# Kernel tuning notes

Hardware: AMD Instinct MI355X
Metric: run time of the kernel (lower is better)

Reference implementation:

```python
import jax, jax.numpy as jnp
import numpy as np

B, L, E, H = 1, 4096, 1024, 16
D = E // H
EPS = 1e-6


def setup_inputs() -> dict:
    key = jax.random.key(0)
    k1, k2, k3 = jax.random.split(key, 3)
    # fan-in scaled init to keep activations sane
    x = jax.random.normal(k1, (B, L, E), dtype=jnp.float32)
    qkv_w = jax.random.normal(k2, (E, 3 * E), dtype=jnp.float32) / np.sqrt(E)
    qkv_b = jnp.zeros((3 * E,), dtype=jnp.float32)
    out_w = jax.random.normal(k3, (E, E), dtype=jnp.float32) / np.sqrt(E)
    out_b = jnp.zeros((E,), dtype=jnp.float32)
    return {"x": x, "qkv_w": qkv_w, "qkv_b": qkv_b, "out_w": out_w, "out_b": out_b}


def reference(x, qkv_w, qkv_b, out_w, out_b):
    b, l, e = x.shape
    qkv = x @ qkv_w + qkv_b                      # (B, L, 3E)
    q, k, v = jnp.split(qkv, 3, axis=-1)
    # (B, L, E) -> (B, H, L, D)
    q = q.reshape(b, l, H, D).transpose(0, 2, 1, 3)
    k = k.reshape(b, l, H, D).transpose(0, 2, 1, 3)
    v = v.reshape(b, l, H, D).transpose(0, 2, 1, 3)
    q_prime = jax.nn.elu(q) + 1.0
    k_prime = jax.nn.elu(k) + 1.0
    # cumulative sum of per-position outer products k'_l v_l^T : (B,H,L,D,D)
    kv_prod = jnp.einsum('bhld,bhle->bhlde', k_prime, v)
    kv_cumsum = jnp.cumsum(kv_prod, axis=2)
    context = jnp.einsum('bhld,bhlde->bhle', q_prime, kv_cumsum)  # (B,H,L,D)
    k_cumsum = jnp.cumsum(k_prime, axis=2)                        # (B,H,L,D)
    norm = jnp.einsum('bhld,bhld->bhl', q_prime, k_cumsum)        # (B,H,L)
    output = context / (norm[..., None] + EPS)
    output = output.transpose(0, 2, 1, 3).reshape(b, l, e)
    return output @ out_w + out_b
```

## Files before the change

### kernel.cpp

```cpp
#include <hip/hip_runtime.h>
#include <cstddef>
#include <cstdint>

#define L_SEQ 4096
#define EMB   1024
#define NH    16
#define HD    64
#define N3    3072
#define CHUNK 64
#define NCHUNK 64
#define EPS 1e-6f

typedef __attribute__((ext_vector_type(8))) short   bf16x8;
typedef __attribute__((ext_vector_type(4))) short   bf16x4;
typedef __attribute__((ext_vector_type(4))) float   floatx4;

#define AS1 __attribute__((address_space(1)))
#define AS3 __attribute__((address_space(3)))

__device__ __forceinline__ void gload_lds16(const void* g, void* l) {
    __builtin_amdgcn_global_load_lds((AS1 const unsigned int*)g,
                                     (AS3 unsigned int*)l, 16, 0, 0);
}

__device__ __forceinline__ short f2bf(float f) {
    union { float f; unsigned u; } a; a.f = f;
    unsigned r = a.u + 0x7fffu + ((a.u >> 16) & 1u);
    return (short)(r >> 16);
}
__device__ __forceinline__ float bf2f(short s) {
    union { unsigned u; float f; } a; a.u = ((unsigned)(unsigned short)s) << 16;
    return a.f;
}

__device__ __forceinline__ void transpose_tile(const float* __restrict__ W,
                                               short* __restrict__ WT,
                                               int K, int N, int bx, int by,
                                               float (*t)[65], int tid)
{
    const int r  = tid >> 4;
    const int c4 = (tid & 15) << 2;
#pragma unroll
    for (int s = 0; s < 4; ++s) {
        const int k = r + s * 16;
        const floatx4 v = *(const floatx4*)&W[(size_t)(by * 64 + k) * N + bx * 64 + c4];
        t[k][c4 + 0] = v[0]; t[k][c4 + 1] = v[1];
        t[k][c4 + 2] = v[2]; t[k][c4 + 3] = v[3];
    }
    __syncthreads();
#pragma unroll
    for (int s = 0; s < 4; ++s) {
        const int n = r + s * 16;
        bf16x4 o;
        o[0] = f2bf(t[c4 + 0][n]); o[1] = f2bf(t[c4 + 1][n]);
        o[2] = f2bf(t[c4 + 2][n]); o[3] = f2bf(t[c4 + 3][n]);
        *(bf16x4*)&WT[(size_t)(bx * 64 + n) * K + by * 64 + c4] = o;
    }
}

__global__ __launch_bounds__(256)
void prep(const float* __restrict__ x, short* __restrict__ xb,
          const float* __restrict__ qkv_w, short* __restrict__ qwt,
          const float* __restrict__ out_w, short* __restrict__ owt)
{
    __shared__ float t[64][65];
    const int b = blockIdx.x;
    const int tid = threadIdx.x;
    if (b < 2048) {
        const int i = b * 256 + tid;
        const floatx4 a = *(const floatx4*)(x + (size_t)i * 8);
        const floatx4 c = *(const floatx4*)(x + (size_t)i * 8 + 4);
        bf16x8 o;
        o[0] = f2bf(a[0]); o[1] = f2bf(a[1]); o[2] = f2bf(a[2]); o[3] = f2bf(a[3]);
        o[4] = f2bf(c[0]); o[5] = f2bf(c[1]); o[6] = f2bf(c[2]); o[7] = f2bf(c[3]);
        *(bf16x8*)(xb + (size_t)i * 8) = o;
    } else if (b < 2048 + 768) {
        const int u = b - 2048;
        transpose_tile(qkv_w, qwt, EMB, N3, u % 48, u / 48, t, tid);
    } else {
        const int u = b - 2816;
        transpose_tile(out_w, owt, EMB, EMB, u & 15, u >> 4, t, tid);
    }
}

#define CST 136

template<int MODE>
__global__ __launch_bounds__(256)
void mfma_gemm(const short* __restrict__ A, const short* __restrict__ BT,
               const float* __restrict__ bias,
               short* __restrict__ OQ, short* __restrict__ OK, short* __restrict__ OV,
               float* __restrict__ OF, int N, int K)
{
    __shared__ __align__(16) short smem[128 * CST];
    short* Asm = smem;
    short* Bsm = smem + 4096;
    const int tid  = threadIdx.x;
    const int lane = tid & 63;
    const int wave = tid >> 6;
    const int wm = (wave >> 1) * 64;
    const int wn = (wave & 1) * 64;
    const int bx = blockIdx.x;
    const int by = blockIdx.y;
    const int frow = lane & 15;
    const int fko  = (lane >> 4) << 3;

    const short* Ab = A  + (size_t)(by * 128) * K;
    const short* Bb = BT + (size_t)(bx * 128) * K;

    floatx4 acc[4][4] = {};

    for (int k0 = 0; k0 < K; k0 += 32) {
#pragma unroll
        for (int q = 0; q < 2; ++q) {
            const int ia = q * 256 + tid;
            const int row = ia >> 2;
            const int kc  = (ia & 3) << 3;
            gload_lds16(Ab + (size_t)row * K + k0 + kc, &Asm[ia << 3]);
            gload_lds16(Bb + (size_t)row * K + k0 + kc, &Bsm[ia << 3]);
        }
        __syncthreads();
        bf16x8 af[4], bfv[4];
#pragma unroll
        for (int mi = 0; mi < 4; ++mi)
            af[mi] = *(const bf16x8*)&Asm[(wm + mi * 16 + frow) * 32 + fko];
#pragma unroll
        for (int ni = 0; ni < 4; ++ni)
            bfv[ni] = *(const bf16x8*)&Bsm[(wn + ni * 16 + frow) * 32 + fko];
#pragma unroll
        for (int mi = 0; mi < 4; ++mi)
#pragma unroll
            for (int ni = 0; ni < 4; ++ni)
                acc[mi][ni] = __builtin_amdgcn_mfma_f32_16x16x32_bf16(
                    af[mi], bfv[ni], acc[mi][ni], 0, 0, 0);
        __syncthreads();
    }

    const int rq = (lane >> 4) << 2;
    if (MODE == 0) {
#pragma unroll
        for (int ni = 0; ni < 4; ++ni) {
            const int n = bx * 128 + wn + ni * 16 + frow;
            const float bv = bias[n];
            const bool do_elu = (n >> 10) < 2;
#pragma unroll
            for (int mi = 0; mi < 4; ++mi)
#pragma unroll
                for (int r = 0; r < 4; ++r) {
                    float v = acc[mi][ni][r] + bv;
                    if (do_elu) v = (v > 0.f) ? (v + 1.f) : __expf(v);
                    smem[(wm + mi * 16 + rq + r) * CST + wn + ni * 16 + frow] = f2bf(v);
                }
        }
        __syncthreads();
#pragma unroll
        for (int t = 0; t < 8; ++t) {
            const int idx = t * 256 + tid;
            const int mm = idx >> 4;
            const int c8 = (idx & 15) << 3;
            const bf16x8 val = *(const bf16x8*)&smem[mm * CST + c8];
            const int n0 = bx * 128 + c8;
            const int rsel = n0 >> 10;
            const int h  = (n0 & 1023) >> 6;
            const int d  = n0 & 63;
            short* base = (rsel == 0) ? OQ : (rsel == 1 ? OK : OV);
            *(bf16x8*)&base[((size_t)(h * L_SEQ + by * 128 + mm)) * HD + d] = val;
        }
    } else {
#pragma unroll
        for (int ni = 0; ni < 4; ++ni) {
            const int n = bx * 128 + wn + ni * 16 + frow;
            const float bv = bias[n];
#pragma unroll
            for (int mi = 0; mi < 4; ++mi)
#pragma unroll
                for (int r = 0; r < 4; ++r) {
                    const int m = by * 128 + wm + mi * 16 + rq + r;
                    OF[(size_t)m * N + n] = acc[mi][ni][r] + bv;
                }
        }
    }
}

__global__ __launch_bounds__(256)
void chunk_state(const short* __restrict__ Kb, const short* __restrict__ Vb,
                 short* __restrict__ ScTb, float* __restrict__ zc)
{
    __shared__ float Kc[CHUNK * HD];
    __shared__ float Vc[CHUNK * HD];
    const int c = blockIdx.x, h = blockIdx.y;
    const int tid = threadIdx.x;
    const short* Kg = Kb + ((size_t)h * L_SEQ + (size_t)c * CHUNK) * HD;
    const short* Vg = Vb + ((size_t)h * L_SEQ + (size_t)c * CHUNK) * HD;
#pragma unroll
    for (int q = 0; q < 2; ++q) {
        const int idx = q * 256 + tid;
        const bf16x8 kv = *(const bf16x8*)&Kg[idx * 8];
        const bf16x8 vv = *(const bf16x8*)&Vg[idx * 8];
#pragma unroll
        for (int j = 0; j < 8; ++j) {
            Kc[idx * 8 + j] = bf2f(kv[j]);
            Vc[idx * 8 + j] = bf2f(vv[j]);
        }
    }
    __syncthreads();
    const int e0 = (tid >> 4) << 2;
    const int d0 = (tid & 15) << 2;
    float acc[4][4] = {{0.f}};
    for (int l = 0; l < CHUNK; ++l) {
        const floatx4 ve = *(const floatx4*)&Vc[l * HD + e0];
        const floatx4 kd = *(const floatx4*)&Kc[l * HD + d0];
#pragma unroll
        for (int a = 0; a < 4; ++a)
#pragma unroll
            for (int b = 0; b < 4; ++b)
                acc[a][b] += ve[a] * kd[b];
    }
    short* Sout = ScTb + (size_t)(h * NCHUNK + c) * 4096;
#pragma unroll
    for (int a = 0; a < 4; ++a) {
        bf16x4 o;
        o[0] = f2bf(acc[a][0]); o[1] = f2bf(acc[a][1]);
        o[2] = f2bf(acc[a][2]); o[3] = f2bf(acc[a][3]);
        *(bf16x4*)&Sout[(e0 + a) * HD + d0] = o;
    }
    if (tid < HD) {
        float z = 0.f;
        for (int l = 0; l < CHUNK; ++l) z += Kc[l * HD + tid];
        zc[((size_t)(h * NCHUNK + c)) * HD + tid] = z;
    }
}

__global__ __launch_bounds__(256)
void prefix_scan(const short* __restrict__ ScTb, const float* __restrict__ zc,
                 short* __restrict__ S0b)
{
    const int g = blockIdx.x * 256 + threadIdx.x;
    const int h  = g >> 12;
    const int ed = g & 4095;
    const int e  = ed >> 6;
    const int d  = ed & 63;
    const short* src = ScTb + (size_t)h * NCHUNK * 4096 + ed;
    float run = 0.f;
    for (int cb = 0; cb < NCHUNK; cb += 8) {
        short v[8];
#pragma unroll
        for (int u = 0; u < 8; ++u) v[u] = src[(size_t)(cb + u) * 4096];
#pragma unroll
        for (int u = 0; u < 8; ++u) {
            S0b[((size_t)((h * NCHUNK + cb + u) * 65 + e)) * 64 + d] = f2bf(run);
            run += bf2f(v[u]);
        }
    }
    if (g < NH * HD) {
        const int h2 = g >> 6, d2 = g & 63;
        float rz = 0.f;
        for (int cb = 0; cb < NCHUNK; cb += 8) {
            float w[8];
#pragma unroll
            for (int u = 0; u < 8; ++u)
                w[u] = zc[((size_t)(h2 * NCHUNK + cb + u)) * HD + d2];
#pragma unroll
            for (int u = 0; u < 8; ++u) {
                S0b[((size_t)((h2 * NCHUNK + cb + u) * 65 + 64)) * 64 + d2] = f2bf(rz);
                rz += w[u];
            }
        }
    }
}

#define SP 72

__global__ __launch_bounds__(256)
void chunk_attn(const short* __restrict__ Qb, const short* __restrict__ Kb,
                const short* __restrict__ Vb, const short* __restrict__ S0b,
                short* __restrict__ attn)
{
    __shared__ __align__(16) short Qs[64 * SP];
    __shared__ __align__(16) short Ks[64 * SP];
    __shared__ __align__(16) short As[64 * SP];
    __shared__ __align__(16) short Vs[80 * SP];
    __shared__ __align__(16) short Ss[80 * SP];
    const int c = blockIdx.x, h = blockIdx.y;
    const int tid = threadIdx.x, lane = tid & 63, wave = tid >> 6;
    const size_t rb = ((size_t)h * L_SEQ + (size_t)c * CHUNK) * HD;
    const short* Qg = Qb + rb;
    const short* Kg = Kb + rb;
    const short* Vg = Vb + rb;
    const short* Sg = S0b + (size_t)(h * NCHUNK + c) * 65 * 64;

#pragma unroll
    for (int q = 0; q < 2; ++q) {
        const int idx = q * 256 + tid;
        const int row = idx >> 3, c8 = (idx & 7) << 3;
        *(bf16x8*)&Qs[row * SP + c8] = *(const bf16x8*)&Qg[row * 64 + c8];
        *(bf16x8*)&Ks[row * SP + c8] = *(const bf16x8*)&Kg[row * 64 + c8];
        const bf16x8 vv = *(const bf16x8*)&Vg[row * 64 + c8];
#pragma unroll
        for (int j = 0; j < 8; ++j) Vs[(c8 + j) * SP + row] = vv[j];
    }
    if (tid < 64) Vs[64 * SP + tid] = (short)0x3F80;
    for (int idx = tid; idx < 520; idx += 256) {
        const int row = idx >> 3, c8 = (idx & 7) << 3;
        *(bf16x8*)&Ss[row * SP + c8] = *(const bf16x8*)&Sg[row * 64 + c8];
    }
    __syncthreads();

    const int frow = lane & 15;
    const int quad = lane >> 4;
    const int fko  = quad << 3;
    const int wm   = wave << 4;

    const bf16x8 qf0 = *(const bf16x8*)&Qs[(wm + frow) * SP + fko];
    const bf16x8 qf1 = *(const bf16x8*)&Qs[(wm + frow) * SP + 32 + fko];

    floatx4 sacc[4] = {};
#pragma unroll
    for (int n = 0; n < 4; ++n) {
        const bf16x8 kf0 = *(const bf16x8*)&Ks[(n * 16 + frow) * SP + fko];
        const bf16x8 kf1 = *(const bf16x8*)&Ks[(n * 16 + frow) * SP + 32 + fko];
        sacc[n] = __builtin_amdgcn_mfma_f32_16x16x32_bf16(qf0, kf0, sacc[n], 0, 0, 0);
        sacc[n] = __builtin_amdgcn_mfma_f32_16x16x32_bf16(qf1, kf1, sacc[n], 0, 0, 0);
    }
#pragma unroll
    for (int n = 0; n < 4; ++n)
#pragma unroll
        for (int r = 0; r < 4; ++r) {
            const int i = wm + quad * 4 + r;
            const int j = n * 16 + frow;
            As[i * SP + j] = (j <= i) ? f2bf(sacc[n][r]) : (short)0;
        }
    __syncthreads();

    const bf16x8 af0 = *(const bf16x8*)&As[(wm + frow) * SP + fko];
    const bf16x8 af1 = *(const bf16x8*)&As[(wm + frow) * SP + 32 + fko];
    floatx4 oacc[5] = {};
#pragma unroll
    for (int n = 0; n < 5; ++n) {
        const bf16x8 vf0 = *(const bf16x8*)&Vs[(n * 16 + frow) * SP + fko];
        const bf16x8 vf1 = *(const bf16x8*)&Vs[(n * 16 + frow) * SP + 32 + fko];
        oacc[n] = __builtin_amdgcn_mfma_f32_16x16x32_bf16(af0, vf0, oacc[n], 0, 0, 0);
        oacc[n] = __builtin_amdgcn_mfma_f32_16x16x32_bf16(af1, vf1, oacc[n], 0, 0, 0);
        const bf16x8 sf0 = *(const bf16x8*)&Ss[(n * 16 + frow) * SP + fko];
        const bf16x8 sf1 = *(const bf16x8*)&Ss[(n * 16 + frow) * SP + 32 + fko];
        oacc[n] = __builtin_amdgcn_mfma_f32_16x16x32_bf16(qf0, sf0, oacc[n], 0, 0, 0);
        oacc[n] = __builtin_amdgcn_mfma_f32_16x16x32_bf16(qf1, sf1, oacc[n], 0, 0, 0);
    }

#pragma unroll
    for (int r = 0; r < 4; ++r) {
        const float norm = __shfl(oacc[4][r], lane & 48) + EPS;
        const float inv = 1.f / norm;
        const int i = wm + quad * 4 + r;
#pragma unroll
        for (int n = 0; n < 4; ++n)
            As[i * SP + n * 16 + frow] = f2bf(oacc[n][r] * inv);
    }
    __syncthreads();
#pragma unroll
    for (int t = 0; t < 2; ++t) {
        const int idx = t * 256 + tid;
        const int row = idx >> 3, c8 = (idx & 7) << 3;
        *(bf16x8*)&attn[(size_t)(c * CHUNK + row) * EMB + h * HD + c8] =
            *(const bf16x8*)&As[row * SP + c8];
    }
}

extern "C" void kernel_launch(void* const* d_in, const int* in_sizes, int n_in,
                              void* d_out, int out_size, void* d_ws, size_t ws_size,
                              hipStream_t stream)
{
    const float* x     = (const float*)d_in[0];
    const float* qkv_w = (const float*)d_in[1];
    const float* qkv_b = (const float*)d_in[2];
    const float* out_w = (const float*)d_in[3];
    const float* out_b = (const float*)d_in[4];
    float* out = (float*)d_out;

    short* ws    = (short*)d_ws;
    short* Qb    = ws;
    short* Kb    = Qb + 4194304;
    short* Vb    = Kb + 4194304;
    short* xb    = Vb + 4194304;
    short* qwt   = xb + 4194304;
    short* owt   = qwt + 3145728;
    short* attnb = owt + 1048576;
    short* S0b   = attnb + 4194304;
    short* ScTb  = S0b + 4259840;
    float* zc    = (float*)(ScTb + 4194304);

    prep<<<dim3(3072), 256, 0, stream>>>(x, xb, qkv_w, qwt, out_w, owt);
    mfma_gemm<0><<<dim3(N3 / 128, L_SEQ / 128), 256, 0, stream>>>(
        xb, qwt, qkv_b, Qb, Kb, Vb, nullptr, N3, EMB);
    chunk_state<<<dim3(NCHUNK, NH), 256, 0, stream>>>(Kb, Vb, ScTb, zc);
    prefix_scan<<<dim3((NH * 4096) / 256), 256, 0, stream>>>(ScTb, zc, S0b);
    chunk_attn<<<dim3(NCHUNK, NH), 256, 0, stream>>>(Qb, Kb, Vb, S0b, attnb);
    mfma_gemm<1><<<dim3(EMB / 128, L_SEQ / 128), 256, 0, stream>>>(
        attnb, owt, out_b, nullptr, nullptr, nullptr, out, EMB, EMB);
}
```

Baseline: 179.9 us.

## Fuse prefix scan into chunk attention and retile both GEMMs with K=64 steps

Removes the separate prefix_scan kernel. Each chunk_attn block now sums the previous chunk states and key sums from ScTb/zc directly, which cuts one launch and the S0b round trip but adds O(c) redundant reads per block, quadratic in chunk count. Both GEMMs now stage two 32-wide K panels per barrier, halving the synchronisations. The output GEMM uses 64-row tiles to double its block count and improve occupancy on 1024x4096.

```diff
diff --git a/kernel.cpp b/kernel.cpp
--- a/kernel.cpp
+++ b/kernel.cpp
@@ -85,16 +85,14 @@
 
 #define CST 136
 
-template<int MODE>
 __global__ __launch_bounds__(256)
-void mfma_gemm(const short* __restrict__ A, const short* __restrict__ BT,
-               const float* __restrict__ bias,
-               short* __restrict__ OQ, short* __restrict__ OK, short* __restrict__ OV,
-               float* __restrict__ OF, int N, int K)
+void mfma_gemm_qkv(const short* __restrict__ A, const short* __restrict__ BT,
+                   const float* __restrict__ bias,
+                   short* __restrict__ OQ, short* __restrict__ OK,
+                   short* __restrict__ OV, int N, int K)
 {
     __shared__ __align__(16) short smem[128 * CST];
-    short* Asm = smem;
-    short* Bsm = smem + 4096;
+    short* pan[4] = { smem, smem + 4096, smem + 8192, smem + 12288 };
     const int tid  = threadIdx.x;
     const int lane = tid & 63;
     const int wave = tid >> 6;
@@ -103,82 +101,150 @@
     const int bx = blockIdx.x;
     const int by = blockIdx.y;
     const int frow = lane & 15;
-    const int fko  = (lane >> 4) << 3;
+    const int quad = lane >> 4;
+    const int fko  = quad << 3;
 
     const short* Ab = A  + (size_t)(by * 128) * K;
     const short* Bb = BT + (size_t)(bx * 128) * K;
 
     floatx4 acc[4][4] = {};
 
-    for (int k0 = 0; k0 < K; k0 += 32) {
-#pragma unroll
-        for (int q = 0; q < 2; ++q) {
-            const int ia = q * 256 + tid;
-            const int row = ia >> 2;
-            const int kc  = (ia & 3) << 3;
-            gload_lds16(Ab + (size_t)row * K + k0 + kc, &Asm[ia << 3]);
-            gload_lds16(Bb + (size_t)row * K + k0 + kc, &Bsm[ia << 3]);
+    for (int k0 = 0; k0 < K; k0 += 64) {
+#pragma unroll
+        for (int p = 0; p < 2; ++p) {
+            const int kp = k0 + p * 32;
+#pragma unroll
+            for (int q = 0; q < 2; ++q) {
+                const int ia = q * 256 + tid;
+                const int row = ia >> 2;
+                const int kc  = (ia & 3) << 3;
+                gload_lds16(Ab + (size_t)row * K + kp + kc, &pan[p * 2 + 0][ia << 3]);
+                gload_lds16(Bb + (size_t)row * K + kp + kc, &pan[p * 2 + 1][ia << 3]);
+            }
         }
         __syncthreads();
-        bf16x8 af[4], bfv[4];
+#pragma unroll
+        for (int p = 0; p < 2; ++p) {
+            bf16x8 af[4], bfv[4];
+#pragma unroll
+            for (int mi = 0; mi < 4; ++mi)
+                af[mi] = *(const bf16x8*)&pan[p * 2 + 0][(wm + mi * 16 + frow) * 32 + fko];
+#pragma unroll
+            for (int ni = 0; ni < 4; ++ni)
+                bfv[ni] = *(const bf16x8*)&pan[p * 2 + 1][(wn + ni * 16 + frow) * 32 + fko];
+#pragma unroll
+            for (int mi = 0; mi < 4; ++mi)
+#pragma unroll
+                for (int ni = 0; ni < 4; ++ni)
+                    acc[mi][ni] = __builtin_amdgcn_mfma_f32_16x16x32_bf16(
+                        af[mi], bfv[ni], acc[mi][ni], 0, 0, 0);
+        }
+        __syncthreads();
+    }
+
+    const int rq = quad << 2;
+#pragma unroll
+    for (int ni = 0; ni < 4; ++ni) {
+        const int n = bx * 128 + wn + ni * 16 + frow;
+        const float bv = bias[n];
+        const bool do_elu = (n >> 10) < 2;
 #pragma unroll
         for (int mi = 0; mi < 4; ++mi)
-            af[mi] = *(const bf16x8*)&Asm[(wm + mi * 16 + frow) * 32 + fko];
-#pragma unroll
-        for (int ni = 0; ni < 4; ++ni)
-            bfv[ni] = *(const bf16x8*)&Bsm[(wn + ni * 16 + frow) * 32 + fko];
-#pragma unroll
-        for (int mi = 0; mi < 4; ++mi)
+#pragma unroll
+            for (int r = 0; r < 4; ++r) {
+                float v = acc[mi][ni][r] + bv;
+                if (do_elu) v = (v > 0.f) ? (v + 1.f) : __expf(v);
+                smem[(wm + mi * 16 + rq + r) * CST + wn + ni * 16 + frow] = f2bf(v);
+            }
+    }
+    __syncthreads();
+#pragma unroll
+    for (int t = 0; t < 8; ++t) {
+        const int idx = t * 256 + tid;
+        const int mm = idx >> 4;
+        const int c8 = (idx & 15) << 3;
+        const bf16x8 val = *(const bf16x8*)&smem[mm * CST + c8];
+        const int n0 = bx * 128 + c8;
+        const int rsel = n0 >> 10;
+        const int h  = (n0 & 1023) >> 6;
+        const int d  = n0 & 63;
+        short* base = (rsel == 0) ? OQ : (rsel == 1 ? OK : OV);
+        *(bf16x8*)&base[((size_t)(h * L_SEQ + by * 128 + mm)) * HD + d] = val;
+    }
+}
+
+__global__ __launch_bounds__(256)
+void mfma_gemm_out(const short* __restrict__ A, const short* __restrict__ BT,
+                   const float* __restrict__ bias, float* __restrict__ OF,
+                   int N, int K)
+{
+    __shared__ __align__(16) short smem[12288];
+    short* pan[4] = { smem, smem + 2048, smem + 6144, smem + 8192 };
+    const int tid  = threadIdx.x;
+    const int lane = tid & 63;
+    const int wave = tid >> 6;
+    const int wm = (wave >> 1) * 32;
+    const int wn = (wave & 1) * 64;
+    const int bx = blockIdx.x;
+    const int by = blockIdx.y;
+    const int frow = lane & 15;
+    const int quad = lane >> 4;
+    const int fko  = quad << 3;
+
+    const short* Ab = A  + (size_t)(by * 64) * K;
+    const short* Bb = BT + (size_t)(bx * 128) * K;
+
+    floatx4 acc[2][4] = {};
+
+    for (int k0 = 0; k0 < K; k0 += 64) {
+#pragma unroll
+        for (int p = 0; p < 2; ++p) {
+            const int kp = k0 + p * 32;
+            {
+                const int row = tid >> 2;
+                const int kc  = (tid & 3) << 3;
+                gload_lds16(Ab + (size_t)row * K + kp + kc, &pan[p * 2 + 0][tid << 3]);
+            }
+#pragma unroll
+            for (int q = 0; q < 2; ++q) {
+                const int ib = q * 256 + tid;
+                const int row = ib >> 2;
+                const int kc  = (ib & 3) << 3;
+                gload_lds16(Bb + (size_t)row * K + kp + kc, &pan[p * 2 + 1][ib << 3]);
+            }
+        }
+        __syncthreads();
+#pragma unroll
+        for (int p = 0; p < 2; ++p) {
+            bf16x8 af[2], bfv[4];
+#pragma unroll
+            for (int mi = 0; mi < 2; ++mi)
+                af[mi] = *(const bf16x8*)&pan[p * 2 + 0][(wm + mi * 16 + frow) * 32 + fko];
 #pragma unroll
             for (int ni = 0; ni < 4; ++ni)
-                acc[mi][ni] = __builtin_amdgcn_mfma_f32_16x16x32_bf16(
-                    af[mi], bfv[ni], acc[mi][ni], 0, 0, 0);
+                bfv[ni] = *(const bf16x8*)&pan[p * 2 + 1][(wn + ni * 16 + frow) * 32 + fko];
+#pragma unroll
+            for (int mi = 0; mi < 2; ++mi)
+#pragma unroll
+                for (int ni = 0; ni < 4; ++ni)
+                    acc[mi][ni] = __builtin_amdgcn_mfma_f32_16x16x32_bf16(
+                        af[mi], bfv[ni], acc[mi][ni], 0, 0, 0);
+        }
         __syncthreads();
     }
 
-    const int rq = (lane >> 4) << 2;
-    if (MODE == 0) {
-#pragma unroll
-        for (int ni = 0; ni < 4; ++ni) {
-            const int n = bx * 128 + wn + ni * 16 + frow;
-            const float bv = bias[n];
-            const bool do_elu = (n >> 10) < 2;
-#pragma unroll
-            for (int mi = 0; mi < 4; ++mi)
-#pragma unroll
-                for (int r = 0; r < 4; ++r) {
-                    float v = acc[mi][ni][r] + bv;
-                    if (do_elu) v = (v > 0.f) ? (v + 1.f) : __expf(v);
-                    smem[(wm + mi * 16 + rq + r) * CST + wn + ni * 16 + frow] = f2bf(v);
-                }
-        }
-        __syncthreads();
-#pragma unroll
-        for (int t = 0; t < 8; ++t) {
-            const int idx = t * 256 + tid;
-            const int mm = idx >> 4;
-            const int c8 = (idx & 15) << 3;
-            const bf16x8 val = *(const bf16x8*)&smem[mm * CST + c8];
-            const int n0 = bx * 128 + c8;
-            const int rsel = n0 >> 10;
-            const int h  = (n0 & 1023) >> 6;
-            const int d  = n0 & 63;
-            short* base = (rsel == 0) ? OQ : (rsel == 1 ? OK : OV);
-            *(bf16x8*)&base[((size_t)(h * L_SEQ + by * 128 + mm)) * HD + d] = val;
-        }
-    } else {
-#pragma unroll
-        for (int ni = 0; ni < 4; ++ni) {
-            const int n = bx * 128 + wn + ni * 16 + frow;
-            const float bv = bias[n];
-#pragma unroll
-            for (int mi = 0; mi < 4; ++mi)
-#pragma unroll
-                for (int r = 0; r < 4; ++r) {
-                    const int m = by * 128 + wm + mi * 16 + rq + r;
-                    OF[(size_t)m * N + n] = acc[mi][ni][r] + bv;
-                }
-        }
+    const int rq = quad << 2;
+#pragma unroll
+    for (int ni = 0; ni < 4; ++ni) {
+        const int n = bx * 128 + wn + ni * 16 + frow;
+        const float bv = bias[n];
+#pragma unroll
+        for (int mi = 0; mi < 2; ++mi)
+#pragma unroll
+            for (int r = 0; r < 4; ++r) {
+                const int m = by * 64 + wm + mi * 16 + rq + r;
+                OF[(size_t)m * N + n] = acc[mi][ni][r] + bv;
+            }
     }
 }
 
@@ -231,50 +297,12 @@
     }
 }
 
-__global__ __launch_bounds__(256)
-void prefix_scan(const short* __restrict__ ScTb, const float* __restrict__ zc,
-                 short* __restrict__ S0b)
-{
-    const int g = blockIdx.x * 256 + threadIdx.x;
-    const int h  = g >> 12;
-    const int ed = g & 4095;
-    const int e  = ed >> 6;
-    const int d  = ed & 63;
-    const short* src = ScTb + (size_t)h * NCHUNK * 4096 + ed;
-    float run = 0.f;
-    for (int cb = 0; cb < NCHUNK; cb += 8) {
-        short v[8];
-#pragma unroll
-        for (int u = 0; u < 8; ++u) v[u] = src[(size_t)(cb + u) * 4096];
-#pragma unroll
-        for (int u = 0; u < 8; ++u) {
-            S0b[((size_t)((h * NCHUNK + cb + u) * 65 + e)) * 64 + d] = f2bf(run);
-            run += bf2f(v[u]);
-        }
-    }
-    if (g < NH * HD) {
-        const int h2 = g >> 6, d2 = g & 63;
-        float rz = 0.f;
-        for (int cb = 0; cb < NCHUNK; cb += 8) {
-            float w[8];
-#pragma unroll
-            for (int u = 0; u < 8; ++u)
-                w[u] = zc[((size_t)(h2 * NCHUNK + cb + u)) * HD + d2];
-#pragma unroll
-            for (int u = 0; u < 8; ++u) {
-                S0b[((size_t)((h2 * NCHUNK + cb + u) * 65 + 64)) * 64 + d2] = f2bf(rz);
-                rz += w[u];
-            }
-        }
-    }
-}
-
 #define SP 72
 
 __global__ __launch_bounds__(256)
 void chunk_attn(const short* __restrict__ Qb, const short* __restrict__ Kb,
-                const short* __restrict__ Vb, const short* __restrict__ S0b,
-                short* __restrict__ attn)
+                const short* __restrict__ Vb, const short* __restrict__ ScTb,
+                const float* __restrict__ zc, short* __restrict__ attn)
 {
     __shared__ __align__(16) short Qs[64 * SP];
     __shared__ __align__(16) short Ks[64 * SP];
@@ -287,7 +315,6 @@
     const short* Qg = Qb + rb;
     const short* Kg = Kb + rb;
     const short* Vg = Vb + rb;
-    const short* Sg = S0b + (size_t)(h * NCHUNK + c) * 65 * 64;
 
 #pragma unroll
     for (int q = 0; q < 2; ++q) {
@@ -300,9 +327,31 @@
         for (int j = 0; j < 8; ++j) Vs[(c8 + j) * SP + row] = vv[j];
     }
     if (tid < 64) Vs[64 * SP + tid] = (short)0x3F80;
-    for (int idx = tid; idx < 520; idx += 256) {
-        const int row = idx >> 3, c8 = (idx & 7) << 3;
-        *(bf16x8*)&Ss[row * SP + c8] = *(const bf16x8*)&Sg[row * 64 + c8];
+
+    {
+        const int ed0 = tid * 16;
+        const int e = ed0 >> 6, d0 = ed0 & 63;
+        float s[16];
+#pragma unroll
+        for (int j = 0; j < 16; ++j) s[j] = 0.f;
+        const short* Sp = ScTb + (size_t)(h * NCHUNK) * 4096 + ed0;
+        for (int c2 = 0; c2 < c; ++c2) {
+            const bf16x8 a = *(const bf16x8*)(Sp + (size_t)c2 * 4096);
+            const bf16x8 b = *(const bf16x8*)(Sp + (size_t)c2 * 4096 + 8);
+#pragma unroll
+            for (int j = 0; j < 8; ++j) { s[j] += bf2f(a[j]); s[8 + j] += bf2f(b[j]); }
+        }
+        bf16x8 o0, o1;
+#pragma unroll
+        for (int j = 0; j < 8; ++j) { o0[j] = f2bf(s[j]); o1[j] = f2bf(s[8 + j]); }
+        *(bf16x8*)&Ss[e * SP + d0]     = o0;
+        *(bf16x8*)&Ss[e * SP + d0 + 8] = o1;
+    }
+    if (tid < 64) {
+        float z = 0.f;
+        const float* zp = zc + (size_t)(h * NCHUNK) * 64 + tid;
+        for (int c2 = 0; c2 < c; ++c2) z += zp[(size_t)c2 * 64];
+        Ss[64 * SP + tid] = f2bf(z);
     }
     __syncthreads();
 
@@ -385,16 +434,14 @@
     short* qwt   = xb + 4194304;
     short* owt   = qwt + 3145728;
     short* attnb = owt + 1048576;
-    short* S0b   = attnb + 4194304;
-    short* ScTb  = S0b + 4259840;
+    short* ScTb  = attnb + 4194304;
     float* zc    = (float*)(ScTb + 4194304);
 
     prep<<<dim3(3072), 256, 0, stream>>>(x, xb, qkv_w, qwt, out_w, owt);
-    mfma_gemm<0><<<dim3(N3 / 128, L_SEQ / 128), 256, 0, stream>>>(
-        xb, qwt, qkv_b, Qb, Kb, Vb, nullptr, N3, EMB);
+    mfma_gemm_qkv<<<dim3(N3 / 128, L_SEQ / 128), 256, 0, stream>>>(
+        xb, qwt, qkv_b, Qb, Kb, Vb, N3, EMB);
     chunk_state<<<dim3(NCHUNK, NH), 256, 0, stream>>>(Kb, Vb, ScTb, zc);
-    prefix_scan<<<dim3((NH * 4096) / 256), 256, 0, stream>>>(ScTb, zc, S0b);
-    chunk_attn<<<dim3(NCHUNK, NH), 256, 0, stream>>>(Qb, Kb, Vb, S0b, attnb);
-    mfma_gemm<1><<<dim3(EMB / 128, L_SEQ / 128), 256, 0, stream>>>(
-        attnb, owt, out_b, nullptr, nullptr, nullptr, out, EMB, EMB);
-}
+    chunk_attn<<<dim3(NCHUNK, NH), 256, 0, stream>>>(Qb, Kb, Vb, ScTb, zc, attnb);
+    mfma_gemm_out<<<dim3(EMB / 128, L_SEQ / 64), 256, 0, stream>>>(
+        attnb, owt, out_b, out, EMB, EMB);
+}
```

Result: slower. 196.6 us (+9.3%).
